# Optimization experiments

Measured on AMD Instinct MI355X. Metric: run time of the kernel, lower is better.

## Reference

```python
import jax, jax.numpy as jnp
import numpy as np

RADIUS = 11.0  # init kwarg
N, D = 8192, 64


def setup_inputs() -> dict:
    key = jax.random.key(0)
    kx, ka = jax.random.split(key)
    x = jax.random.normal(kx, (N, D), dtype=jnp.float32)
    adj = jax.random.randint(ka, (N, 16), 0, N, dtype=jnp.int32)  # unused by the layer
    return {"x": x, "adj": adj}


def reference(x, adj):
    # Pairwise Euclidean distances via Gram trick (same math as
    # sqrt(sum((x_i - x_j)^2)) but avoids materializing the [N, N, D] diff).
    sq = jnp.sum(x * x, axis=-1)                       # [N]
    d2 = sq[:, None] + sq[None, :] - 2.0 * (x @ x.T)    # [N, N]
    distances = jnp.sqrt(jnp.maximum(d2, 0.0))          # [N, N]
    mask = (distances <= RADIUS).astype(x.dtype)        # binary ball-query mask
    attention_scores = jax.nn.softmax(mask, axis=-1)    # softmax over 0/1 scores
    return attention_scores @ x                          # [N, D]
```

## Files before the change

### kernel.cpp

```cpp
#include <hip/hip_runtime.h>
#include <hip/hip_bf16.h>


#define NROWS 8192

typedef __bf16 bf16x8 __attribute__((ext_vector_type(8)));
typedef float  f32x4  __attribute__((ext_vector_type(4)));
typedef unsigned int u32;
typedef u32 u32x4 __attribute__((ext_vector_type(4)));

#define MFMA16(A, B, C) __builtin_amdgcn_mfma_f32_16x16x32_bf16((A), (B), (C), 0, 0, 0)

#define GLOAD16(g, l)                                                     \
    __builtin_amdgcn_global_load_lds(                                     \
        (const __attribute__((address_space(1))) u32*)(g),                \
        (__attribute__((address_space(3))) u32*)(l), 16, 0, 0)

static __device__ __forceinline__ unsigned short bf16rn(float f) {
    unsigned u = __float_as_uint(f);
    unsigned r = u + 0x7FFFu + ((u >> 16) & 1u);
    return (unsigned short)(r >> 16);
}
static __device__ __forceinline__ float bf16tof(unsigned short h) {
    return __uint_as_float(((unsigned)h) << 16);
}

__global__ __launch_bounds__(256) void prep(const float* __restrict__ x,
                                            unsigned short* __restrict__ xhi,
                                            unsigned short* __restrict__ xlo,
                                            float* __restrict__ sq,
                                            float* __restrict__ stot) {
    __shared__ float sp[4][64];
    int t = blockIdx.x * 256 + threadIdx.x;
    int row = t >> 4, q = t & 15;
    const float4 v = *(const float4*)(x + ((size_t)row << 6) + (q << 2));
    float f0 = v.x, f1 = v.y, f2 = v.z, f3 = v.w;
    unsigned short h0 = bf16rn(f0), h1 = bf16rn(f1), h2 = bf16rn(f2), h3 = bf16rn(f3);
    unsigned short l0 = bf16rn(f0 - bf16tof(h0));
    unsigned short l1 = bf16rn(f1 - bf16tof(h1));
    unsigned short l2 = bf16rn(f2 - bf16tof(h2));
    unsigned short l3 = bf16rn(f3 - bf16tof(h3));
    uint2 ph, pl;
    ph.x = (u32)h0 | ((u32)h1 << 16);  ph.y = (u32)h2 | ((u32)h3 << 16);
    pl.x = (u32)l0 | ((u32)l1 << 16);  pl.y = (u32)l2 | ((u32)l3 << 16);
    *(uint2*)(xhi + ((size_t)row << 6) + (q << 2)) = ph;
    *(uint2*)(xlo + ((size_t)row << 6) + (q << 2)) = pl;
    float ss = f0 * f0;
    ss = fmaf(f1, f1, ss); ss = fmaf(f2, f2, ss); ss = fmaf(f3, f3, ss);
    ss += __shfl_xor(ss, 1); ss += __shfl_xor(ss, 2);
    ss += __shfl_xor(ss, 4); ss += __shfl_xor(ss, 8);
    if (q == 0) sq[row] = ss;
    f0 += __shfl_xor(f0, 16); f0 += __shfl_xor(f0, 32);
    f1 += __shfl_xor(f1, 16); f1 += __shfl_xor(f1, 32);
    f2 += __shfl_xor(f2, 16); f2 += __shfl_xor(f2, 32);
    f3 += __shfl_xor(f3, 16); f3 += __shfl_xor(f3, 32);
    int l = threadIdx.x & 63, wv = threadIdx.x >> 6;
    if (l < 16) {
        sp[wv][l * 4 + 0] = f0; sp[wv][l * 4 + 1] = f1;
        sp[wv][l * 4 + 2] = f2; sp[wv][l * 4 + 3] = f3;
    }
    __syncthreads();
    if (threadIdx.x < 64) {
        float s = sp[0][threadIdx.x] + sp[1][threadIdx.x] +
                  sp[2][threadIdx.x] + sp[3][threadIdx.x];
        atomicAdd(stot + threadIdx.x, s);
    }
}

static __device__ __forceinline__ int jslot(int j) {
    return (j & 32) | (((j >> 2) & 3) << 3) | (((j >> 4) & 1) << 2) | (j & 3);
}

__global__ __launch_bounds__(256, 3) void ballq_main(
        const unsigned short* __restrict__ xhi,
        const unsigned short* __restrict__ xlo,
        const float* __restrict__ sq,
        float* __restrict__ S, float* __restrict__ cnt) {
    __shared__ char sHI[2][8192];
    __shared__ char sLO[2][8192];
    __shared__ char sJT[2][8192];
    __shared__ float sqJ[2][64];

    const int tid = threadIdx.x;
    const int w = tid >> 6, l = tid & 63, l16 = l & 15, lg = l >> 4;
    const int itile = blockIdx.x & 63, chunk = blockIdx.x >> 6;
    const int i0 = (itile << 7) + w * 32;
    const int jt0 = chunk * 10 + (chunk < 8 ? chunk : 8);
    const int jtn = (chunk < 8) ? 11 : 10;

    const int srow = l >> 3;
    const int schunk = (l & 7) ^ srow;
    const size_t gsoff = ((size_t)srow << 6) + (schunk << 3);

    const int sj = (tid & 31) * 2;
    const int sd0 = (tid >> 5) * 8;
    const int sslot2 = jslot(sj) * 2;

    bf16x8 ihi[2][2], ilo[2][2];
    float sqi[2];
#pragma unroll
    for (int mt = 0; mt < 2; ++mt) {
        int ir = i0 + mt * 16 + l16;
#pragma unroll
        for (int ks = 0; ks < 2; ++ks) {
            size_t off = (size_t)ir * 64 + ks * 32 + lg * 8;
            ihi[mt][ks] = *(const bf16x8*)(xhi + off);
            ilo[mt][ks] = *(const bf16x8*)(xlo + off);
        }
        sqi[mt] = sq[ir];
    }

    f32x4 accS[2][4];
    u32 pcnt[2] = {0u, 0u};
#pragma unroll
    for (int a = 0; a < 2; ++a)
#pragma unroll
        for (int b = 0; b < 4; ++b) {
            accS[a][b][0] = 0.f; accS[a][b][1] = 0.f;
            accS[a][b][2] = 0.f; accS[a][b][3] = 0.f;
        }

    {
        int j0 = jt0 << 6;
        const unsigned short* gh = xhi + ((size_t)(j0 + w * 16) << 6) + gsoff;
        const unsigned short* gl = xlo + ((size_t)(j0 + w * 16) << 6) + gsoff;
        GLOAD16(gh,       &sHI[0][w * 16 * 128]);
        GLOAD16(gh + 512, &sHI[0][(w * 16 + 8) * 128]);
        GLOAD16(gl,       &sLO[0][w * 16 * 128]);
        GLOAD16(gl + 512, &sLO[0][(w * 16 + 8) * 128]);
        uint4 h0 = *(const uint4*)(xhi + (size_t)(j0 + sj) * 64 + sd0);
        uint4 h1 = *(const uint4*)(xhi + (size_t)(j0 + sj + 1) * 64 + sd0);
        float sqv = (tid < 64) ? sq[j0 + tid] : 0.f;
        const unsigned short* a0 = (const unsigned short*)&h0;
        const unsigned short* a1 = (const unsigned short*)&h1;
#pragma unroll
        for (int e = 0; e < 8; ++e) {
            u32 pv = (u32)a0[e] | ((u32)a1[e] << 16);
            *(u32*)(sJT[0] + (sd0 + e) * 128 + (sslot2 ^ (e << 4))) = pv;
        }
        if (tid < 64) sqJ[0][tid] = sqv;
    }
    __syncthreads();

    const int csw = (lg ^ (l16 & 7)) << 4;
    int buf = 0;
    for (int t = 0; t < jtn; ++t) {
        const bool more = (t + 1 < jtn);
        uint4 n0, n1; float nsq = 0.f;
        if (more) {
            int jn = (jt0 + t + 1) << 6;
            const unsigned short* gh = xhi + ((size_t)(jn + w * 16) << 6) + gsoff;
            const unsigned short* gl = xlo + ((size_t)(jn + w * 16) << 6) + gsoff;
            char* hb = sHI[buf ^ 1];
            char* lb = sLO[buf ^ 1];
            GLOAD16(gh,       hb + w * 16 * 128);
            GLOAD16(gh + 512, hb + (w * 16 + 8) * 128);
            GLOAD16(gl,       lb + w * 16 * 128);
            GLOAD16(gl + 512, lb + (w * 16 + 8) * 128);
            n0 = *(const uint4*)(xhi + (size_t)(jn + sj) * 64 + sd0);
            n1 = *(const uint4*)(xhi + (size_t)(jn + sj + 1) * 64 + sd0);
            if (tid < 64) nsq = sq[jn + tid];
        }

        const char* hb = sHI[buf];
        const char* lb = sLO[buf];
        f32x4 accD[4][2];
#pragma unroll
        for (int a = 0; a < 4; ++a)
#pragma unroll
            for (int b = 0; b < 2; ++b) {
                accD[a][b][0] = 0.f; accD[a][b][1] = 0.f;
                accD[a][b][2] = 0.f; accD[a][b][3] = 0.f;
            }
#pragma unroll
        for (int nt = 0; nt < 4; ++nt) {
            const int ro = (nt * 16 + l16) * 128;
            bf16x8 jh[2], jl[2];
            jh[0] = *(const bf16x8*)(hb + ro + csw);
            jh[1] = *(const bf16x8*)(hb + ro + (csw ^ 64));
            jl[0] = *(const bf16x8*)(lb + ro + csw);
            jl[1] = *(const bf16x8*)(lb + ro + (csw ^ 64));
#pragma unroll
            for (int mt = 0; mt < 2; ++mt)
#pragma unroll
                for (int ks = 0; ks < 2; ++ks) {
                    accD[nt][mt] = MFMA16(jh[ks], ihi[mt][ks], accD[nt][mt]);
                    accD[nt][mt] = MFMA16(jh[ks], ilo[mt][ks], accD[nt][mt]);
                    accD[nt][mt] = MFMA16(jl[ks], ihi[mt][ks], accD[nt][mt]);
                }
        }

        u32 Fw[2][8];
#pragma unroll
        for (int nt = 0; nt < 4; ++nt) {
            const int kj = nt >> 1, s = nt & 1;
            f32x4 sqr = *(const f32x4*)&sqJ[buf][nt * 16 + lg * 4];
#pragma unroll
            for (int mt = 0; mt < 2; ++mt) {
                float base = sqi[mt];
                bool in0 = fmaf(-2.f, accD[nt][mt][0], base + sqr[0]) <= 121.f;
                bool in1 = fmaf(-2.f, accD[nt][mt][1], base + sqr[1]) <= 121.f;
                bool in2 = fmaf(-2.f, accD[nt][mt][2], base + sqr[2]) <= 121.f;
                bool in3 = fmaf(-2.f, accD[nt][mt][3], base + sqr[3]) <= 121.f;
                Fw[mt][kj * 4 + s * 2 + 0] =
                    (in0 ? 0x3F80u : 0u) | (in1 ? 0x3F800000u : 0u);
                Fw[mt][kj * 4 + s * 2 + 1] =
                    (in2 ? 0x3F80u : 0u) | (in3 ? 0x3F800000u : 0u);
            }
        }
#pragma unroll
        for (int mt = 0; mt < 2; ++mt)
#pragma unroll
            for (int wd = 0; wd < 8; ++wd)
                pcnt[mt] += (u32)__builtin_popcount(Fw[mt][wd]);

#pragma unroll
        for (int kj = 0; kj < 2; ++kj) {
            u32x4 fa0 = {Fw[0][kj * 4 + 0], Fw[0][kj * 4 + 1],
                         Fw[0][kj * 4 + 2], Fw[0][kj * 4 + 3]};
            u32x4 fa1 = {Fw[1][kj * 4 + 0], Fw[1][kj * 4 + 1],
                         Fw[1][kj * 4 + 2], Fw[1][kj * 4 + 3]};
            bf16x8 m0 = __builtin_bit_cast(bf16x8, fa0);
            bf16x8 m1 = __builtin_bit_cast(bf16x8, fa1);
#pragma unroll
            for (int ntd = 0; ntd < 4; ++ntd) {
                const char* bp = sJT[buf] + (ntd * 16 + l16) * 128 +
                                 ((kj * 64 + lg * 16) ^ ((l16 & 7) << 4));
                bf16x8 bT = *(const bf16x8*)bp;
                accS[0][ntd] = MFMA16(m0, bT, accS[0][ntd]);
                accS[1][ntd] = MFMA16(m1, bT, accS[1][ntd]);
            }
        }

        if (more) {
            char* jb = sJT[buf ^ 1];
            const unsigned short* a0 = (const unsigned short*)&n0;
            const unsigned short* a1 = (const unsigned short*)&n1;
#pragma unroll
            for (int e = 0; e < 8; ++e) {
                u32 pv = (u32)a0[e] | ((u32)a1[e] << 16);
                *(u32*)(jb + (sd0 + e) * 128 + (sslot2 ^ (e << 4))) = pv;
            }
            if (tid < 64) sqJ[buf ^ 1][tid] = nsq;
        }
        __syncthreads();
        buf ^= 1;
    }

#pragma unroll
    for (int mt = 0; mt < 2; ++mt) {
        u32 v = pcnt[mt];
        v += __shfl_xor(v, 16);
        v += __shfl_xor(v, 32);
        if (lg == 0) atomicAdd(cnt + i0 + mt * 16 + l16, (float)(v / 7u));
    }
#pragma unroll
    for (int mt = 0; mt < 2; ++mt)
#pragma unroll
        for (int ntd = 0; ntd < 4; ++ntd)
#pragma unroll
            for (int r = 0; r < 4; ++r) {
                size_t idx = (size_t)(i0 + mt * 16 + lg * 4 + r) * 64 + ntd * 16 + l16;
                atomicAdd(S + idx, accS[mt][ntd][r]);
            }
}

__global__ __launch_bounds__(256) void ballq_combine(
        const float* __restrict__ S, const float* __restrict__ cnt,
        const float* __restrict__ stot, float* __restrict__ out) {
    int t = blockIdx.x * 256 + threadIdx.x;
    int i = t >> 4, d0 = (t & 15) << 2;
    float c = cnt[i];
    f32x4 s = *(const f32x4*)(S + (size_t)i * 64 + d0);
    f32x4 st = *(const f32x4*)(stot + d0);
    const float K = 0.36787944117144233f;
    float den = 1.f / (c + K * (8192.f - c));
    f32x4 o;
#pragma unroll
    for (int k = 0; k < 4; ++k) o[k] = (s[k] + K * (st[k] - s[k])) * den;
    *(f32x4*)(out + (size_t)i * 64 + d0) = o;
}

extern "C" void kernel_launch(void* const* d_in, const int* in_sizes, int n_in,
                              void* d_out, int out_size, void* d_ws, size_t ws_size,
                              hipStream_t stream) {
    (void)in_sizes; (void)n_in; (void)out_size; (void)ws_size;
    const float* x = (const float*)d_in[0];
    float* out = (float*)d_out;
    char* ws = (char*)d_ws;

    unsigned short* xhi = (unsigned short*)ws;
    unsigned short* xlo = (unsigned short*)(ws + (1u << 20));
    float* sq   = (float*)(ws + (2u << 20));
    float* S    = (float*)(ws + (2u << 20) + 32768);
    float* cnt  = (float*)(ws + (2u << 20) + 32768 + (1u << 21));
    float* stot = (float*)(ws + (2u << 20) + 32768 + (1u << 21) + 32768);

    hipMemsetAsync(S, 0, (1u << 21) + 32768 + 256, stream);
    prep<<<512, 256, 0, stream>>>(x, xhi, xlo, sq, stot);
    ballq_main<<<64 * 12, 256, 0, stream>>>(xhi, xlo, sq, S, cnt);
    ballq_combine<<<512, 256, 0, stream>>>(S, cnt, stot, out);
}
```

Baseline: 119.4 us.

## Enlarge per-wave i-tile to 64 rows, fold memset and column-sum into kernels

Each wave now handles 64 query rows instead of 32, so every j-tile loaded into LDS is reused across four MFMA row tiles. The grid becomes 32 i-tiles by 16 equal j-chunks, which removes the uneven chunk split, and occupancy is lowered to 2 blocks per CU to make room for the extra registers. The hipMemsetAsync is replaced by zeroing S and cnt inside prep. The column-sum atomics move from prep into chunk-0 blocks of the main kernel as per-tile partials, which the combine kernel reduces. The tradeoff is higher register pressure and fewer blocks (512 instead of 768), and the column sum is now taken from the hi+lo bf16 split rather than the exact fp32 values.

```diff
diff --git a/kernel.cpp b/kernel.cpp
--- a/kernel.cpp
+++ b/kernel.cpp
@@ -3,6 +3,8 @@
 
 
 #define NROWS 8192
+#define NCHUNK 16
+#define JPT 8
 
 typedef __bf16 bf16x8 __attribute__((ext_vector_type(8)));
 typedef float  f32x4  __attribute__((ext_vector_type(4)));
@@ -29,8 +31,8 @@
                                             unsigned short* __restrict__ xhi,
                                             unsigned short* __restrict__ xlo,
                                             float* __restrict__ sq,
-                                            float* __restrict__ stot) {
-    __shared__ float sp[4][64];
+                                            float* __restrict__ S,
+                                            float* __restrict__ cnt) {
     int t = blockIdx.x * 256 + threadIdx.x;
     int row = t >> 4, q = t & 15;
     const float4 v = *(const float4*)(x + ((size_t)row << 6) + (q << 2));
@@ -50,43 +52,32 @@
     ss += __shfl_xor(ss, 1); ss += __shfl_xor(ss, 2);
     ss += __shfl_xor(ss, 4); ss += __shfl_xor(ss, 8);
     if (q == 0) sq[row] = ss;
-    f0 += __shfl_xor(f0, 16); f0 += __shfl_xor(f0, 32);
-    f1 += __shfl_xor(f1, 16); f1 += __shfl_xor(f1, 32);
-    f2 += __shfl_xor(f2, 16); f2 += __shfl_xor(f2, 32);
-    f3 += __shfl_xor(f3, 16); f3 += __shfl_xor(f3, 32);
-    int l = threadIdx.x & 63, wv = threadIdx.x >> 6;
-    if (l < 16) {
-        sp[wv][l * 4 + 0] = f0; sp[wv][l * 4 + 1] = f1;
-        sp[wv][l * 4 + 2] = f2; sp[wv][l * 4 + 3] = f3;
-    }
-    __syncthreads();
-    if (threadIdx.x < 64) {
-        float s = sp[0][threadIdx.x] + sp[1][threadIdx.x] +
-                  sp[2][threadIdx.x] + sp[3][threadIdx.x];
-        atomicAdd(stot + threadIdx.x, s);
-    }
+    f32x4 z = {0.f, 0.f, 0.f, 0.f};
+    ((f32x4*)S)[t] = z;
+    if (t < 2048) ((f32x4*)cnt)[t] = z;
 }
 
 static __device__ __forceinline__ int jslot(int j) {
     return (j & 32) | (((j >> 2) & 3) << 3) | (((j >> 4) & 1) << 2) | (j & 3);
 }
 
-__global__ __launch_bounds__(256, 3) void ballq_main(
+__global__ __launch_bounds__(256, 2) void ballq_main(
         const unsigned short* __restrict__ xhi,
         const unsigned short* __restrict__ xlo,
         const float* __restrict__ sq,
-        float* __restrict__ S, float* __restrict__ cnt) {
+        float* __restrict__ S, float* __restrict__ cnt,
+        float* __restrict__ stotp) {
     __shared__ char sHI[2][8192];
     __shared__ char sLO[2][8192];
     __shared__ char sJT[2][8192];
     __shared__ float sqJ[2][64];
+    __shared__ float stcol[64];
 
     const int tid = threadIdx.x;
     const int w = tid >> 6, l = tid & 63, l16 = l & 15, lg = l >> 4;
-    const int itile = blockIdx.x & 63, chunk = blockIdx.x >> 6;
-    const int i0 = (itile << 7) + w * 32;
-    const int jt0 = chunk * 10 + (chunk < 8 ? chunk : 8);
-    const int jtn = (chunk < 8) ? 11 : 10;
+    const int itile = blockIdx.x & 31, chunk = blockIdx.x >> 5;
+    const int i0 = (itile << 8) + w * 64;
+    const int jt0 = chunk * JPT;
 
     const int srow = l >> 3;
     const int schunk = (l & 7) ^ srow;
@@ -96,10 +87,10 @@
     const int sd0 = (tid >> 5) * 8;
     const int sslot2 = jslot(sj) * 2;
 
-    bf16x8 ihi[2][2], ilo[2][2];
-    float sqi[2];
-#pragma unroll
-    for (int mt = 0; mt < 2; ++mt) {
+    bf16x8 ihi[4][2], ilo[4][2];
+    float sqi[4];
+#pragma unroll
+    for (int mt = 0; mt < 4; ++mt) {
         int ir = i0 + mt * 16 + l16;
 #pragma unroll
         for (int ks = 0; ks < 2; ++ks) {
@@ -110,10 +101,40 @@
         sqi[mt] = sq[ir];
     }
 
-    f32x4 accS[2][4];
-    u32 pcnt[2] = {0u, 0u};
-#pragma unroll
-    for (int a = 0; a < 2; ++a)
+    if (chunk == 0) {
+        if (tid < 64) stcol[tid] = 0.f;
+        __syncthreads();
+        float sv[2][8];
+#pragma unroll
+        for (int ks = 0; ks < 2; ++ks)
+#pragma unroll
+            for (int e = 0; e < 8; ++e) {
+                float s = 0.f;
+#pragma unroll
+                for (int mt = 0; mt < 4; ++mt) {
+                    const unsigned short* hp = (const unsigned short*)&ihi[mt][ks];
+                    const unsigned short* lp = (const unsigned short*)&ilo[mt][ks];
+                    s += bf16tof(hp[e]) + bf16tof(lp[e]);
+                }
+                s += __shfl_xor(s, 1); s += __shfl_xor(s, 2);
+                s += __shfl_xor(s, 4); s += __shfl_xor(s, 8);
+                sv[ks][e] = s;
+            }
+        if (l16 == 0) {
+#pragma unroll
+            for (int ks = 0; ks < 2; ++ks)
+#pragma unroll
+                for (int e = 0; e < 8; ++e)
+                    atomicAdd(&stcol[ks * 32 + lg * 8 + e], sv[ks][e]);
+        }
+        __syncthreads();
+        if (tid < 64) stotp[itile * 64 + tid] = stcol[tid];
+    }
+
+    f32x4 accS[4][4];
+    u32 pcnt[4] = {0u, 0u, 0u, 0u};
+#pragma unroll
+    for (int a = 0; a < 4; ++a)
 #pragma unroll
         for (int b = 0; b < 4; ++b) {
             accS[a][b][0] = 0.f; accS[a][b][1] = 0.f;
@@ -144,19 +165,19 @@
 
     const int csw = (lg ^ (l16 & 7)) << 4;
     int buf = 0;
-    for (int t = 0; t < jtn; ++t) {
-        const bool more = (t + 1 < jtn);
+    for (int t = 0; t < JPT; ++t) {
+        const bool more = (t + 1 < JPT);
         uint4 n0, n1; float nsq = 0.f;
         if (more) {
             int jn = (jt0 + t + 1) << 6;
             const unsigned short* gh = xhi + ((size_t)(jn + w * 16) << 6) + gsoff;
             const unsigned short* gl = xlo + ((size_t)(jn + w * 16) << 6) + gsoff;
-            char* hb = sHI[buf ^ 1];
-            char* lb = sLO[buf ^ 1];
-            GLOAD16(gh,       hb + w * 16 * 128);
-            GLOAD16(gh + 512, hb + (w * 16 + 8) * 128);
-            GLOAD16(gl,       lb + w * 16 * 128);
-            GLOAD16(gl + 512, lb + (w * 16 + 8) * 128);
+            char* hb2 = sHI[buf ^ 1];
+            char* lb2 = sLO[buf ^ 1];
+            GLOAD16(gh,       hb2 + w * 16 * 128);
+            GLOAD16(gh + 512, hb2 + (w * 16 + 8) * 128);
+            GLOAD16(gl,       lb2 + w * 16 * 128);
+            GLOAD16(gl + 512, lb2 + (w * 16 + 8) * 128);
             n0 = *(const uint4*)(xhi + (size_t)(jn + sj) * 64 + sd0);
             n1 = *(const uint4*)(xhi + (size_t)(jn + sj + 1) * 64 + sd0);
             if (tid < 64) nsq = sq[jn + tid];
@@ -164,14 +185,7 @@
 
         const char* hb = sHI[buf];
         const char* lb = sLO[buf];
-        f32x4 accD[4][2];
-#pragma unroll
-        for (int a = 0; a < 4; ++a)
-#pragma unroll
-            for (int b = 0; b < 2; ++b) {
-                accD[a][b][0] = 0.f; accD[a][b][1] = 0.f;
-                accD[a][b][2] = 0.f; accD[a][b][3] = 0.f;
-            }
+        u32 Fw[4][8];
 #pragma unroll
         for (int nt = 0; nt < 4; ++nt) {
             const int ro = (nt * 16 + l16) * 128;
@@ -180,55 +194,58 @@
             jh[1] = *(const bf16x8*)(hb + ro + (csw ^ 64));
             jl[0] = *(const bf16x8*)(lb + ro + csw);
             jl[1] = *(const bf16x8*)(lb + ro + (csw ^ 64));
-#pragma unroll
-            for (int mt = 0; mt < 2; ++mt)
-#pragma unroll
-                for (int ks = 0; ks < 2; ++ks) {
-                    accD[nt][mt] = MFMA16(jh[ks], ihi[mt][ks], accD[nt][mt]);
-                    accD[nt][mt] = MFMA16(jh[ks], ilo[mt][ks], accD[nt][mt]);
-                    accD[nt][mt] = MFMA16(jl[ks], ihi[mt][ks], accD[nt][mt]);
+            f32x4 accD[4];
+#pragma unroll
+            for (int a = 0; a < 4; ++a) {
+                accD[a][0] = 0.f; accD[a][1] = 0.f;
+                accD[a][2] = 0.f; accD[a][3] = 0.f;
+            }
+#pragma unroll
+            for (int ks = 0; ks < 2; ++ks)
+#pragma unroll
+                for (int mt = 0; mt < 4; ++mt) {
+                    accD[mt] = MFMA16(jh[ks], ihi[mt][ks], accD[mt]);
+                    accD[mt] = MFMA16(jh[ks], ilo[mt][ks], accD[mt]);
+                    accD[mt] = MFMA16(jl[ks], ihi[mt][ks], accD[mt]);
                 }
-        }
-
-        u32 Fw[2][8];
-#pragma unroll
-        for (int nt = 0; nt < 4; ++nt) {
-            const int kj = nt >> 1, s = nt & 1;
+            const int kj = nt >> 1, s2 = (nt & 1) * 2;
             f32x4 sqr = *(const f32x4*)&sqJ[buf][nt * 16 + lg * 4];
 #pragma unroll
-            for (int mt = 0; mt < 2; ++mt) {
+            for (int mt = 0; mt < 4; ++mt) {
                 float base = sqi[mt];
-                bool in0 = fmaf(-2.f, accD[nt][mt][0], base + sqr[0]) <= 121.f;
-                bool in1 = fmaf(-2.f, accD[nt][mt][1], base + sqr[1]) <= 121.f;
-                bool in2 = fmaf(-2.f, accD[nt][mt][2], base + sqr[2]) <= 121.f;
-                bool in3 = fmaf(-2.f, accD[nt][mt][3], base + sqr[3]) <= 121.f;
-                Fw[mt][kj * 4 + s * 2 + 0] =
+                bool in0 = fmaf(-2.f, accD[mt][0], base + sqr[0]) <= 121.f;
+                bool in1 = fmaf(-2.f, accD[mt][1], base + sqr[1]) <= 121.f;
+                bool in2 = fmaf(-2.f, accD[mt][2], base + sqr[2]) <= 121.f;
+                bool in3 = fmaf(-2.f, accD[mt][3], base + sqr[3]) <= 121.f;
+                Fw[mt][kj * 4 + s2 + 0] =
                     (in0 ? 0x3F80u : 0u) | (in1 ? 0x3F800000u : 0u);
-                Fw[mt][kj * 4 + s * 2 + 1] =
+                Fw[mt][kj * 4 + s2 + 1] =
                     (in2 ? 0x3F80u : 0u) | (in3 ? 0x3F800000u : 0u);
             }
         }
 #pragma unroll
-        for (int mt = 0; mt < 2; ++mt)
+        for (int mt = 0; mt < 4; ++mt)
 #pragma unroll
             for (int wd = 0; wd < 8; ++wd)
                 pcnt[mt] += (u32)__builtin_popcount(Fw[mt][wd]);
 
 #pragma unroll
         for (int kj = 0; kj < 2; ++kj) {
-            u32x4 fa0 = {Fw[0][kj * 4 + 0], Fw[0][kj * 4 + 1],
-                         Fw[0][kj * 4 + 2], Fw[0][kj * 4 + 3]};
-            u32x4 fa1 = {Fw[1][kj * 4 + 0], Fw[1][kj * 4 + 1],
-                         Fw[1][kj * 4 + 2], Fw[1][kj * 4 + 3]};
-            bf16x8 m0 = __builtin_bit_cast(bf16x8, fa0);
-            bf16x8 m1 = __builtin_bit_cast(bf16x8, fa1);
+            bf16x8 m[4];
+#pragma unroll
+            for (int mt = 0; mt < 4; ++mt) {
+                u32x4 fa = {Fw[mt][kj * 4 + 0], Fw[mt][kj * 4 + 1],
+                            Fw[mt][kj * 4 + 2], Fw[mt][kj * 4 + 3]};
+                m[mt] = __builtin_bit_cast(bf16x8, fa);
+            }
 #pragma unroll
             for (int ntd = 0; ntd < 4; ++ntd) {
                 const char* bp = sJT[buf] + (ntd * 16 + l16) * 128 +
                                  ((kj * 64 + lg * 16) ^ ((l16 & 7) << 4));
                 bf16x8 bT = *(const bf16x8*)bp;
-                accS[0][ntd] = MFMA16(m0, bT, accS[0][ntd]);
-                accS[1][ntd] = MFMA16(m1, bT, accS[1][ntd]);
+#pragma unroll
+                for (int mt = 0; mt < 4; ++mt)
+                    accS[mt][ntd] = MFMA16(m[mt], bT, accS[mt][ntd]);
             }
         }
 
@@ -248,14 +265,14 @@
     }
 
 #pragma unroll
-    for (int mt = 0; mt < 2; ++mt) {
+    for (int mt = 0; mt < 4; ++mt) {
         u32 v = pcnt[mt];
         v += __shfl_xor(v, 16);
         v += __shfl_xor(v, 32);
         if (lg == 0) atomicAdd(cnt + i0 + mt * 16 + l16, (float)(v / 7u));
     }
 #pragma unroll
-    for (int mt = 0; mt < 2; ++mt)
+    for (int mt = 0; mt < 4; ++mt)
 #pragma unroll
         for (int ntd = 0; ntd < 4; ++ntd)
 #pragma unroll
@@ -267,17 +284,25 @@
 
 __global__ __launch_bounds__(256) void ballq_combine(
         const float* __restrict__ S, const float* __restrict__ cnt,
-        const float* __restrict__ stot, float* __restrict__ out) {
+        const float* __restrict__ stotp, float* __restrict__ out) {
+    __shared__ float st[64];
+    if (threadIdx.x < 64) {
+        float s = 0.f;
+#pragma unroll
+        for (int g = 0; g < 32; ++g) s += stotp[g * 64 + threadIdx.x];
+        st[threadIdx.x] = s;
+    }
+    __syncthreads();
     int t = blockIdx.x * 256 + threadIdx.x;
     int i = t >> 4, d0 = (t & 15) << 2;
     float c = cnt[i];
     f32x4 s = *(const f32x4*)(S + (size_t)i * 64 + d0);
-    f32x4 st = *(const f32x4*)(stot + d0);
+    f32x4 stv = *(const f32x4*)&st[d0];
     const float K = 0.36787944117144233f;
     float den = 1.f / (c + K * (8192.f - c));
     f32x4 o;
 #pragma unroll
-    for (int k = 0; k < 4; ++k) o[k] = (s[k] + K * (st[k] - s[k])) * den;
+    for (int k = 0; k < 4; ++k) o[k] = (s[k] + K * (stv[k] - s[k])) * den;
     *(f32x4*)(out + (size_t)i * 64 + d0) = o;
 }
 
@@ -291,13 +316,12 @@
 
     unsigned short* xhi = (unsigned short*)ws;
     unsigned short* xlo = (unsigned short*)(ws + (1u << 20));
-    float* sq   = (float*)(ws + (2u << 20));
-    float* S    = (float*)(ws + (2u << 20) + 32768);
-    float* cnt  = (float*)(ws + (2u << 20) + 32768 + (1u << 21));
-    float* stot = (float*)(ws + (2u << 20) + 32768 + (1u << 21) + 32768);
-
-    hipMemsetAsync(S, 0, (1u << 21) + 32768 + 256, stream);
-    prep<<<512, 256, 0, stream>>>(x, xhi, xlo, sq, stot);
-    ballq_main<<<64 * 12, 256, 0, stream>>>(xhi, xlo, sq, S, cnt);
-    ballq_combine<<<512, 256, 0, stream>>>(S, cnt, stot, out);
-}
+    float* sq    = (float*)(ws + (2u << 20));
+    float* S     = (float*)(ws + (2u << 20) + 32768);
+    float* cnt   = (float*)(ws + (2u << 20) + 32768 + (1u << 21));
+    float* stotp = (float*)(ws + (2u << 20) + 32768 + (1u << 21) + 32768);
+
+    prep<<<512, 256, 0, stream>>>(x, xhi, xlo, sq, S, cnt);
+    ballq_main<<<32 * NCHUNK, 256, 0, stream>>>(xhi, xlo, sq, S, cnt, stotp);
+    ballq_combine<<<512, 256, 0, stream>>>(S, cnt, stotp, out);
+}
```

Result: no change. 120.4 us (+0.9%).
